# Optimization experiments

Hardware: AMD Instinct MI355X
Metric: run time of the kernel (lower is better)

The kernel has to match this reference:

```python
import jax, jax.numpy as jnp
import numpy as np

BITS = 4
N_PACK = 8  # 32-bit container / 4-bit values
GROUP_SIZE = 128
MASK = (1 << BITS) - 1  # 0xF


def setup_inputs() -> dict:
    key = jax.random.key(0)
    k1, k2, k3, k4, k5 = jax.random.split(key, 5)
    in_f, out_f = 4096, 4096
    tokens = 8192
    n_groups = in_f // GROUP_SIZE
    x = jax.random.normal(k1, (tokens, in_f), dtype=jnp.float32)
    qweight = jax.random.randint(k2, (in_f // N_PACK, out_f), 0, 2147483647, dtype=jnp.int32)
    qzeros = jax.random.randint(k3, (n_groups, out_f // N_PACK), 0, 2147483647, dtype=jnp.int32)
    scales = jax.random.uniform(k4, (n_groups, out_f), dtype=jnp.float32) * 0.01 + 1e-3
    bias = jax.random.normal(k5, (out_f,), dtype=jnp.float32)
    return {"x": x, "qweight": qweight, "qzeros": qzeros, "scales": scales, "bias": bias}


def _unpack_rows(q):
    # q: [in/8, out] int32 -> [in, out] nibbles (unpack along dim 0)
    shifts = (jnp.arange(N_PACK, dtype=jnp.int32) * BITS)  # [8]
    w = (q[:, None, :] >> shifts[None, :, None]) & MASK    # [in/8, 8, out]
    return w.reshape(-1, q.shape[1])                       # [in, out]


def _unpack_cols(q):
    # q: [G, out/8] int32 -> [G, out] nibbles (unpack along dim 1)
    shifts = (jnp.arange(N_PACK, dtype=jnp.int32) * BITS)
    z = (q[:, :, None] >> shifts[None, None, :]) & MASK    # [G, out/8, 8]
    return z.reshape(q.shape[0], -1)                       # [G, out]


def reference(x, qweight, qzeros, scales, bias):
    in_f = qweight.shape[0] * N_PACK
    int_w = _unpack_rows(qweight)                 # [in, out] uint nibbles
    zp = _unpack_cols(qzeros) + 1                 # optimum format: zp was stored as zp-1
    g = jnp.arange(in_f) // GROUP_SIZE            # group index per input channel
    # dequantize: W[i, j] = (int_w[i,j] - zp[g(i), j]) * scales[g(i), j]
    W = (int_w.astype(jnp.float32) - zp[g].astype(jnp.float32)) * scales[g]
    return x @ W + bias
```

## Files before the change

kernel.cpp:

```cpp
#include <hip/hip_runtime.h>
#include <hip/hip_bf16.h>
#include <stdint.h>

typedef __bf16 bf8 __attribute__((ext_vector_type(8)));
typedef float  f4  __attribute__((ext_vector_type(4)));

__device__ __forceinline__ unsigned f2bf(float f) {
  union { float f; unsigned u; } v; v.f = f;
  return (v.u + 0x7FFFu + ((v.u >> 16) & 1u)) >> 16;
}

__device__ __forceinline__ void gload_lds16(const void* g, void* l) {
  __builtin_amdgcn_global_load_lds(
      (const __attribute__((address_space(1))) void*)(uintptr_t)g,
      (__attribute__((address_space(3))) void*)(uint32_t)(uintptr_t)l,
      16, 0, 0);
}

__global__ void cvt_x(const float4* __restrict__ x, uint4* __restrict__ xb, int n16) {
  int i = blockIdx.x * blockDim.x + threadIdx.x;
  if (i >= n16) return;
  float4 f0 = x[2 * i], f1 = x[2 * i + 1];
  uint4 w;
  w.x = f2bf(f0.x) | (f2bf(f0.y) << 16);
  w.y = f2bf(f0.z) | (f2bf(f0.w) << 16);
  w.z = f2bf(f1.x) | (f2bf(f1.y) << 16);
  w.w = f2bf(f1.z) | (f2bf(f1.w) << 16);
  xb[i] = w;
}

__global__ void dq_w(const int* __restrict__ qw, const int* __restrict__ qz,
                     const float* __restrict__ sc, unsigned short* __restrict__ wt,
                     int N, int K, int group_size) {
  int id = blockIdx.x * blockDim.x + threadIdx.x;
  int n  = id % N;
  int kb = id / N;
  if (kb >= K / 64) return;
  int g = (kb * 64) / group_size;
  unsigned zq = ((unsigned)qz[g * (N >> 3) + (n >> 3)] >> (4 * (n & 7))) & 0xFu;
  float zs = (float)(int)(zq + 1u);
  float s  = sc[(size_t)g * N + n];
  #pragma unroll
  for (int r = 0; r < 8; ++r) {
    unsigned q = (unsigned)qw[(size_t)(kb * 8 + r) * N + n];
    uint4 w;
    #pragma unroll
    for (int h = 0; h < 4; ++h) {
      float v0 = (float)(int)((q >> (8 * h))     & 0xFu) - zs;
      float v1 = (float)(int)((q >> (8 * h + 4)) & 0xFu) - zs;
      ((unsigned*)&w)[h] = f2bf(v0 * s) | (f2bf(v1 * s) << 16);
    }
    *(uint4*)(wt + (size_t)n * K + kb * 64 + r * 8) = w;
  }
}

#define BM 256
#define BN 256
#define BK 64

__launch_bounds__(512, 2)
__global__ void gemm_8ph(const unsigned short* __restrict__ A,
                         const unsigned short* __restrict__ B,
                         const float* __restrict__ bias,
                         float* __restrict__ out,
                         int M, int N, int K) {
  __shared__ __align__(16) char smem[131072];

  const int nbx = N / BN;
  const int nwg = (M / BM) * nbx;
  const int id  = blockIdx.y * gridDim.x + blockIdx.x;
  const int cpx = nwg >> 3;
  const int swzid = (id & 7) * cpx + (id >> 3);
  const int m0 = (swzid / nbx) * BM;
  const int n0 = (swzid % nbx) * BN;

  const int t    = threadIdx.x;
  const int wid  = t >> 6, lane = t & 63;
  const int wr   = wid >> 2, wc = wid & 3;
  const int lr   = lane & 15, lk = lane >> 4;
  const unsigned loff = (unsigned)(lr * 64 + (((lk + (lr >> 1)) & 3) << 4));

  const int srow = lane >> 2;
  const int scol = (((lane & 3) - (lane >> 3)) & 3) * 8;

  f4 acc[8][4] = {};

  const int nK = K / BK;

#define STAGE_A(tile, h)                                                          \
  {                                                                               \
    const int _tt = (tile);                                                       \
    _Pragma("unroll")                                                             \
    for (int cg = 0; cg < 2; ++cg) {                                              \
      const unsigned short* _src = A + (size_t)(m0 + (h) * 128 + wid * 16 + srow) * K \
                                     + _tt * BK + cg * 32 + scol;                 \
      char* _dst = smem + (_tt & 1) * 65536 + ((((h) * 8 + wid) * 2 + cg) << 10); \
      gload_lds16(_src, _dst);                                                    \
    }                                                                             \
  }
#define STAGE_B(tile, h)                                                          \
  {                                                                               \
    const int _tt = (tile);                                                       \
    _Pragma("unroll")                                                             \
    for (int cg = 0; cg < 2; ++cg) {                                              \
      const unsigned short* _src = B + (size_t)(n0 + (h) * 128 + wid * 16 + srow) * K \
                                     + _tt * BK + cg * 32 + scol;                 \
      char* _dst = smem + (_tt & 1) * 65536 + 32768 +                             \
                   ((((h) * 8 + wid) * 2 + cg) << 10);                            \
      gload_lds16(_src, _dst);                                                    \
    }                                                                             \
  }

  STAGE_B(0, 0); STAGE_B(0, 1);
  STAGE_A(0, 0); STAGE_A(0, 1);
  if (nK > 1) {
    STAGE_B(1, 0); STAGE_B(1, 1);
    asm volatile("s_waitcnt vmcnt(4)" ::: "memory");
  } else {
    asm volatile("s_waitcnt vmcnt(0)" ::: "memory");
  }
  __builtin_amdgcn_s_barrier();
  __builtin_amdgcn_sched_barrier(0);

  bf8 a[4][2], b[4][2];

  for (int kt = 0; kt < nK; ++kt) {
    const char* pA = smem + (kt & 1) * 65536;
    const char* pB = pA + 32768;
    const int ra = wr * 8;
    const int rb = wc * 4;

    if (kt + 1 < nK) STAGE_A(kt + 1, 0);
    #pragma unroll
    for (int mf = 0; mf < 4; ++mf)
      #pragma unroll
      for (int ks = 0; ks < 2; ++ks)
        a[mf][ks] = *(const bf8*)(pA + (unsigned)((((ra + mf) * 2 + ks) << 10)) + loff);
    #pragma unroll
    for (int nf = 0; nf < 2; ++nf)
      #pragma unroll
      for (int ks = 0; ks < 2; ++ks)
        b[nf][ks] = *(const bf8*)(pB + (unsigned)((((rb + nf) * 2 + ks) << 10)) + loff);
    __builtin_amdgcn_s_barrier();
    __builtin_amdgcn_s_setprio(1);
    #pragma unroll
    for (int mf = 0; mf < 4; ++mf)
      #pragma unroll
      for (int nf = 0; nf < 2; ++nf)
        #pragma unroll
        for (int ks = 0; ks < 2; ++ks)
          acc[mf][nf] = __builtin_amdgcn_mfma_f32_16x16x32_bf16(a[mf][ks], b[nf][ks], acc[mf][nf], 0, 0, 0);
    __builtin_amdgcn_s_setprio(0);
    __builtin_amdgcn_s_barrier();

    if (kt + 1 < nK) STAGE_A(kt + 1, 1);
    #pragma unroll
    for (int nf = 2; nf < 4; ++nf)
      #pragma unroll
      for (int ks = 0; ks < 2; ++ks)
        b[nf][ks] = *(const bf8*)(pB + (unsigned)((((rb + nf) * 2 + ks) << 10)) + loff);
    __builtin_amdgcn_s_barrier();
    __builtin_amdgcn_s_setprio(1);
    #pragma unroll
    for (int mf = 0; mf < 4; ++mf)
      #pragma unroll
      for (int nf = 2; nf < 4; ++nf)
        #pragma unroll
        for (int ks = 0; ks < 2; ++ks)
          acc[mf][nf] = __builtin_amdgcn_mfma_f32_16x16x32_bf16(a[mf][ks], b[nf][ks], acc[mf][nf], 0, 0, 0);
    __builtin_amdgcn_s_setprio(0);
    __builtin_amdgcn_s_barrier();

    if (kt + 2 < nK) STAGE_B(kt + 2, 0);
    #pragma unroll
    for (int mf = 0; mf < 4; ++mf)
      #pragma unroll
      for (int ks = 0; ks < 2; ++ks)
        a[mf][ks] = *(const bf8*)(pA + (unsigned)((((ra + 4 + mf) * 2 + ks) << 10)) + loff);
    __builtin_amdgcn_s_barrier();
    __builtin_amdgcn_s_setprio(1);
    #pragma unroll
    for (int mf = 0; mf < 4; ++mf)
      #pragma unroll
      for (int nf = 2; nf < 4; ++nf)
        #pragma unroll
        for (int ks = 0; ks < 2; ++ks)
          acc[4 + mf][nf] = __builtin_amdgcn_mfma_f32_16x16x32_bf16(a[mf][ks], b[nf][ks], acc[4 + mf][nf], 0, 0, 0);
    __builtin_amdgcn_s_setprio(0);
    __builtin_amdgcn_s_barrier();

    if (kt + 2 < nK) {
      STAGE_B(kt + 2, 1);
      asm volatile("s_waitcnt vmcnt(4)" ::: "memory");
    } else {
      asm volatile("s_waitcnt vmcnt(0)" ::: "memory");
    }
    __builtin_amdgcn_s_barrier();
    __builtin_amdgcn_sched_barrier(0);
    __builtin_amdgcn_s_setprio(1);
    #pragma unroll
    for (int mf = 0; mf < 4; ++mf)
      #pragma unroll
      for (int nf = 0; nf < 2; ++nf)
        #pragma unroll
        for (int ks = 0; ks < 2; ++ks)
          acc[4 + mf][nf] = __builtin_amdgcn_mfma_f32_16x16x32_bf16(a[mf][ks], b[nf][ks], acc[4 + mf][nf], 0, 0, 0);
    __builtin_amdgcn_s_setprio(0);
    __builtin_amdgcn_s_barrier();
  }

  #pragma unroll
  for (int ni = 0; ni < 4; ++ni) {
    int col = n0 + wc * 64 + ni * 16 + lr;
    float bv = bias[col];
    #pragma unroll
    for (int mi = 0; mi < 8; ++mi) {
      int row = m0 + wr * 128 + mi * 16 + lk * 4;
      #pragma unroll
      for (int r = 0; r < 4; ++r)
        out[(size_t)(row + r) * N + col] = acc[mi][ni][r] + bv;
    }
  }
#undef STAGE_A
#undef STAGE_B
}

#define FBM 128
#define FBN 128
#define FBK 64
__launch_bounds__(256, 2)
__global__ void woq_gemm(const float* __restrict__ x,
                         const int*   __restrict__ qweight,
                         const int*   __restrict__ qzeros,
                         const float* __restrict__ scales,
                         const float* __restrict__ bias,
                         float*       __restrict__ out,
                         int M, int N, int K) {
  __shared__ unsigned short sA[FBM * FBK];
  __shared__ unsigned short sB[FBN * FBK];
  const int t = threadIdx.x;
  const int n0 = blockIdx.x * FBN, m0 = blockIdx.y * FBM;
  const int wid = t >> 6, lane = t & 63;
  const int wr = wid >> 1, wc = wid & 1;
  const int lr = lane & 15, lk = lane >> 4;
  f4 acc[4][4] = {};
  const int c = t & 127, rbase = t >> 7;
  const int segA = t & 7, rowbA = t >> 3;
  const int nK = K / FBK;
  for (int kt = 0; kt < nK; ++kt) {
    const int k0 = kt * FBK;
    __syncthreads();
    #pragma unroll
    for (int p = 0; p < 4; ++p) {
      int row = rowbA + p * 32;
      const float4* src = (const float4*)(x + (size_t)(m0 + row) * K + k0 + segA * 8);
      float4 f0 = src[0], f1 = src[1];
      uint4 w;
      w.x = f2bf(f0.x) | (f2bf(f0.y) << 16);
      w.y = f2bf(f0.z) | (f2bf(f0.w) << 16);
      w.z = f2bf(f1.x) | (f2bf(f1.y) << 16);
      w.w = f2bf(f1.z) | (f2bf(f1.w) << 16);
      unsigned off = (unsigned)(row * (FBK * 2) + segA * 16) ^ ((row & 7) << 4);
      *(uint4*)((char*)sA + off) = w;
    }
    {
      const int g = k0 >> 7;
      const unsigned zq = (unsigned)qzeros[g * (N >> 3) + ((n0 + c) >> 3)];
      const int   zp = (int)((zq >> (4 * ((n0 + c) & 7))) & 0xFu) + 1;
      const float sc = scales[(size_t)g * N + n0 + c];
      #pragma unroll
      for (int p = 0; p < 4; ++p) {
        int r = rbase + p * 2;
        unsigned uq = (unsigned)qweight[(size_t)(kt * 8 + r) * N + n0 + c];
        uint4 w;
        #pragma unroll
        for (int h = 0; h < 4; ++h) {
          int v0 = (int)((uq >> (8 * h))     & 0xFu) - zp;
          int v1 = (int)((uq >> (8 * h + 4)) & 0xFu) - zp;
          ((unsigned*)&w)[h] = f2bf((float)v0 * sc) | (f2bf((float)v1 * sc) << 16);
        }
        unsigned off = (unsigned)(c * (FBK * 2) + r * 16) ^ ((c & 7) << 4);
        *(uint4*)((char*)sB + off) = w;
      }
    }
    __syncthreads();
    #pragma unroll
    for (int ks = 0; ks < 2; ++ks) {
      bf8 a[4], b[4];
      #pragma unroll
      for (int mi = 0; mi < 4; ++mi) {
        int row = wr * 64 + mi * 16 + lr;
        unsigned off = (unsigned)(row * (FBK * 2) + ks * 64 + lk * 16) ^ ((row & 7) << 4);
        a[mi] = *(const bf8*)((const char*)sA + off);
      }
      #pragma unroll
      for (int ni = 0; ni < 4; ++ni) {
        int rowN = wc * 64 + ni * 16 + lr;
        unsigned off = (unsigned)(rowN * (FBK * 2) + ks * 64 + lk * 16) ^ ((rowN & 7) << 4);
        b[ni] = *(const bf8*)((const char*)sB + off);
      }
      #pragma unroll
      for (int mi = 0; mi < 4; ++mi)
        #pragma unroll
        for (int ni = 0; ni < 4; ++ni)
          acc[mi][ni] = __builtin_amdgcn_mfma_f32_16x16x32_bf16(a[mi], b[ni], acc[mi][ni], 0, 0, 0);
    }
  }
  #pragma unroll
  for (int ni = 0; ni < 4; ++ni) {
    int col = n0 + wc * 64 + ni * 16 + lr;
    float bv = bias[col];
    #pragma unroll
    for (int mi = 0; mi < 4; ++mi) {
      int row = m0 + wr * 64 + mi * 16 + lk * 4;
      #pragma unroll
      for (int r = 0; r < 4; ++r)
        out[(size_t)(row + r) * N + col] = acc[mi][ni][r] + bv;
    }
  }
}

extern "C" void kernel_launch(void* const* d_in, const int* in_sizes, int n_in,
                              void* d_out, int out_size, void* d_ws, size_t ws_size,
                              hipStream_t stream) {
  const float* x  = (const float*)d_in[0];
  const int*   qw = (const int*)d_in[1];
  const int*   qz = (const int*)d_in[2];
  const float* sc = (const float*)d_in[3];
  const float* bs = (const float*)d_in[4];
  float* out = (float*)d_out;

  const int N = in_sizes[4];
  const int K = (int)(((long long)in_sizes[1] * 8) / N);
  const int M = (int)((long long)in_sizes[0] / K);
  const int n_groups   = (int)((long long)in_sizes[3] / N);
  const int group_size = K / n_groups;

  const size_t need = ((size_t)M * K + (size_t)N * K) * 2;
  if (ws_size >= need && (M % BM) == 0 && (N % BN) == 0 && (K % BK) == 0 &&
      ((M / BM) * (N / BN)) % 8 == 0) {
    unsigned short* xb = (unsigned short*)d_ws;
    unsigned short* wt = xb + (size_t)M * K;

    int n16 = M * K / 8;
    cvt_x<<<(n16 + 255) / 256, 256, 0, stream>>>((const float4*)x, (uint4*)xb, n16);

    int ndq = N * (K / 64);
    dq_w<<<(ndq + 255) / 256, 256, 0, stream>>>(qw, qz, sc, wt, N, K, group_size);

    dim3 grid(N / BN, M / BM);
    gemm_8ph<<<grid, 512, 0, stream>>>(xb, wt, bs, out, M, N, K);
  } else {
    dim3 grid(N / FBN, M / FBM);
    woq_gemm<<<grid, 256, 0, stream>>>(x, qw, qz, sc, bs, out, M, N, K);
  }
}
```

Baseline: 301.6 us.

## Overlap LDS fragment reads with MFMA by prefetching next-phase operands

```diff
diff --git a/kernel.cpp b/kernel.cpp
--- a/kernel.cpp
+++ b/kernel.cpp
@@ -59,11 +59,11 @@
 #define BK 64
 
 __launch_bounds__(512, 2)
-__global__ void gemm_8ph(const unsigned short* __restrict__ A,
-                         const unsigned short* __restrict__ B,
-                         const float* __restrict__ bias,
-                         float* __restrict__ out,
-                         int M, int N, int K) {
+__global__ void gemm_owin(const unsigned short* __restrict__ A,
+                          const unsigned short* __restrict__ B,
+                          const float* __restrict__ bias,
+                          float* __restrict__ out,
+                          int M, int N, int K) {
   __shared__ __align__(16) char smem[131072];
 
   const int nbx = N / BN;
@@ -84,8 +84,11 @@
   const int scol = (((lane & 3) - (lane >> 3)) & 3) * 8;
 
   f4 acc[8][4] = {};
+  bf8 aL[4][2], aH[4][2], b01[2][2], b23[2][2];
 
   const int nK = K / BK;
+  const int ra = wr * 8;
+  const int rb = wc * 4;
 
 #define STAGE_A(tile, h)                                                          \
   {                                                                               \
@@ -110,6 +113,7 @@
       gload_lds16(_src, _dst);                                                    \
     }                                                                             \
   }
+#define RD(p, slot) (*(const bf8*)((p) + ((unsigned)(slot) << 10) + loff))
 
   STAGE_B(0, 0); STAGE_B(0, 1);
   STAGE_A(0, 0); STAGE_A(0, 1);
@@ -121,90 +125,101 @@
   }
   __builtin_amdgcn_s_barrier();
   __builtin_amdgcn_sched_barrier(0);
-
-  bf8 a[4][2], b[4][2];
+  {
+    const char* pA = smem;
+    const char* pB = smem + 32768;
+    #pragma unroll
+    for (int mf = 0; mf < 4; ++mf)
+      #pragma unroll
+      for (int ks = 0; ks < 2; ++ks)
+        aL[mf][ks] = RD(pA, (ra + mf) * 2 + ks);
+    #pragma unroll
+    for (int nf = 0; nf < 2; ++nf)
+      #pragma unroll
+      for (int ks = 0; ks < 2; ++ks)
+        b01[nf][ks] = RD(pB, (rb + nf) * 2 + ks);
+  }
 
   for (int kt = 0; kt < nK; ++kt) {
     const char* pA = smem + (kt & 1) * 65536;
     const char* pB = pA + 32768;
-    const int ra = wr * 8;
-    const int rb = wc * 4;
 
     if (kt + 1 < nK) STAGE_A(kt + 1, 0);
-    #pragma unroll
-    for (int mf = 0; mf < 4; ++mf)
+    __builtin_amdgcn_s_setprio(1);
+    #pragma unroll
+    for (int j = 0; j < 2; ++j)
       #pragma unroll
       for (int ks = 0; ks < 2; ++ks)
-        a[mf][ks] = *(const bf8*)(pA + (unsigned)((((ra + mf) * 2 + ks) << 10)) + loff);
-    #pragma unroll
-    for (int nf = 0; nf < 2; ++nf)
-      #pragma unroll
-      for (int ks = 0; ks < 2; ++ks)
-        b[nf][ks] = *(const bf8*)(pB + (unsigned)((((rb + nf) * 2 + ks) << 10)) + loff);
-    __builtin_amdgcn_s_barrier();
-    __builtin_amdgcn_s_setprio(1);
+        b23[j][ks] = RD(pB, (rb + 2 + j) * 2 + ks);
     #pragma unroll
     for (int mf = 0; mf < 4; ++mf)
       #pragma unroll
       for (int nf = 0; nf < 2; ++nf)
         #pragma unroll
         for (int ks = 0; ks < 2; ++ks)
-          acc[mf][nf] = __builtin_amdgcn_mfma_f32_16x16x32_bf16(a[mf][ks], b[nf][ks], acc[mf][nf], 0, 0, 0);
+          acc[mf][nf] = __builtin_amdgcn_mfma_f32_16x16x32_bf16(aL[mf][ks], b01[nf][ks], acc[mf][nf], 0, 0, 0);
     __builtin_amdgcn_s_setprio(0);
     __builtin_amdgcn_s_barrier();
 
     if (kt + 1 < nK) STAGE_A(kt + 1, 1);
-    #pragma unroll
-    for (int nf = 2; nf < 4; ++nf)
+    __builtin_amdgcn_s_setprio(1);
+    #pragma unroll
+    for (int mf = 0; mf < 4; ++mf)
       #pragma unroll
       for (int ks = 0; ks < 2; ++ks)
-        b[nf][ks] = *(const bf8*)(pB + (unsigned)((((rb + nf) * 2 + ks) << 10)) + loff);
-    __builtin_amdgcn_s_barrier();
-    __builtin_amdgcn_s_setprio(1);
-    #pragma unroll
-    for (int mf = 0; mf < 4; ++mf)
-      #pragma unroll
-      for (int nf = 2; nf < 4; ++nf)
-        #pragma unroll
-        for (int ks = 0; ks < 2; ++ks)
-          acc[mf][nf] = __builtin_amdgcn_mfma_f32_16x16x32_bf16(a[mf][ks], b[nf][ks], acc[mf][nf], 0, 0, 0);
+        aH[mf][ks] = RD(pA, (ra + 4 + mf) * 2 + ks);
+    #pragma unroll
+    for (int mf = 0; mf < 4; ++mf)
+      #pragma unroll
+      for (int j = 0; j < 2; ++j)
+        #pragma unroll
+        for (int ks = 0; ks < 2; ++ks)
+          acc[mf][2 + j] = __builtin_amdgcn_mfma_f32_16x16x32_bf16(aL[mf][ks], b23[j][ks], acc[mf][2 + j], 0, 0, 0);
     __builtin_amdgcn_s_setprio(0);
     __builtin_amdgcn_s_barrier();
 
     if (kt + 2 < nK) STAGE_B(kt + 2, 0);
-    #pragma unroll
-    for (int mf = 0; mf < 4; ++mf)
-      #pragma unroll
-      for (int ks = 0; ks < 2; ++ks)
-        a[mf][ks] = *(const bf8*)(pA + (unsigned)((((ra + 4 + mf) * 2 + ks) << 10)) + loff);
-    __builtin_amdgcn_s_barrier();
     __builtin_amdgcn_s_setprio(1);
     #pragma unroll
     for (int mf = 0; mf < 4; ++mf)
       #pragma unroll
-      for (int nf = 2; nf < 4; ++nf)
-        #pragma unroll
-        for (int ks = 0; ks < 2; ++ks)
-          acc[4 + mf][nf] = __builtin_amdgcn_mfma_f32_16x16x32_bf16(a[mf][ks], b[nf][ks], acc[4 + mf][nf], 0, 0, 0);
+      for (int nf = 0; nf < 2; ++nf)
+        #pragma unroll
+        for (int ks = 0; ks < 2; ++ks)
+          acc[4 + mf][nf] = __builtin_amdgcn_mfma_f32_16x16x32_bf16(aH[mf][ks], b01[nf][ks], acc[4 + mf][nf], 0, 0, 0);
     __builtin_amdgcn_s_setprio(0);
-    __builtin_amdgcn_s_barrier();
 
     if (kt + 2 < nK) {
       STAGE_B(kt + 2, 1);
       asm volatile("s_waitcnt vmcnt(4)" ::: "memory");
-    } else {
+    } else if (kt + 1 < nK) {
       asm volatile("s_waitcnt vmcnt(0)" ::: "memory");
     }
     __builtin_amdgcn_s_barrier();
     __builtin_amdgcn_sched_barrier(0);
+
     __builtin_amdgcn_s_setprio(1);
-    #pragma unroll
-    for (int mf = 0; mf < 4; ++mf)
+    if (kt + 1 < nK) {
+      const char* qA = smem + ((kt + 1) & 1) * 65536;
+      const char* qB = qA + 32768;
+      #pragma unroll
+      for (int mf = 0; mf < 4; ++mf)
+        #pragma unroll
+        for (int ks = 0; ks < 2; ++ks)
+          aL[mf][ks] = RD(qA, (ra + mf) * 2 + ks);
       #pragma unroll
       for (int nf = 0; nf < 2; ++nf)
         #pragma unroll
         for (int ks = 0; ks < 2; ++ks)
-          acc[4 + mf][nf] = __builtin_amdgcn_mfma_f32_16x16x32_bf16(a[mf][ks], b[nf][ks], acc[4 + mf][nf], 0, 0, 0);
+          b01[nf][ks] = RD(qB, (rb + nf) * 2 + ks);
+    }
+    #pragma unroll
+    for (int mf = 0; mf < 4; ++mf)
+      #pragma unroll
+      for (int j = 0; j < 2; ++j)
+        #pragma unroll
+        for (int ks = 0; ks < 2; ++ks)
+          acc[4 + mf][2 + j] = __builtin_amdgcn_mfma_f32_16x16x32_bf16(aH[mf][ks], b23[j][ks], acc[4 + mf][2 + j], 0, 0, 0);
     __builtin_amdgcn_s_setprio(0);
     __builtin_amdgcn_s_barrier();
   }
@@ -223,6 +238,7 @@
   }
 #undef STAGE_A
 #undef STAGE_B
+#undef RD
 }
 
 #define FBM 128
@@ -349,7 +365,7 @@
     dq_w<<<(ndq + 255) / 256, 256, 0, stream>>>(qw, qz, sc, wt, N, K, group_size);
 
     dim3 grid(N / BN, M / BM);
-    gemm_8ph<<<grid, 512, 0, stream>>>(xb, wt, bs, out, M, N, K);
+    gemm_owin<<<grid, 512, 0, stream>>>(xb, wt, bs, out, M, N, K);
   } else {
     dim3 grid(N / FBN, M / FBM);
     woq_gemm<<<grid, 256, 0, stream>>>(x, qw, qz, sc, bs, out, M, N, K);
```

Measured after the change: 290.5 us. -3.7%, faster.

## Switch main GEMM to 32x32x16 MFMA with new LDS layout and interleaved schedule

Applied to the files above, without the earlier changes.

```diff
diff --git a/kernel.cpp b/kernel.cpp
--- a/kernel.cpp
+++ b/kernel.cpp
@@ -2,8 +2,9 @@
 #include <hip/hip_bf16.h>
 #include <stdint.h>
 
-typedef __bf16 bf8 __attribute__((ext_vector_type(8)));
-typedef float  f4  __attribute__((ext_vector_type(4)));
+typedef __bf16 bf8  __attribute__((ext_vector_type(8)));
+typedef float  f4   __attribute__((ext_vector_type(4)));
+typedef float  f16v __attribute__((ext_vector_type(16)));
 
 __device__ __forceinline__ unsigned f2bf(float f) {
   union { float f; unsigned u; } v; v.f = f;
@@ -58,12 +59,16 @@
 #define BN 256
 #define BK 64
 
+#define SGB(mask, n) __builtin_amdgcn_sched_group_barrier((mask), (n), 0)
+#define M_MFMA 0x8
+#define M_DSRD 0x100
+
 __launch_bounds__(512, 2)
-__global__ void gemm_8ph(const unsigned short* __restrict__ A,
-                         const unsigned short* __restrict__ B,
-                         const float* __restrict__ bias,
-                         float* __restrict__ out,
-                         int M, int N, int K) {
+__global__ void gemm32(const unsigned short* __restrict__ A,
+                       const unsigned short* __restrict__ B,
+                       const float* __restrict__ bias,
+                       float* __restrict__ out,
+                       int M, int N, int K) {
   __shared__ __align__(16) char smem[131072];
 
   const int nbx = N / BN;
@@ -77,152 +82,154 @@
   const int t    = threadIdx.x;
   const int wid  = t >> 6, lane = t & 63;
   const int wr   = wid >> 2, wc = wid & 3;
-  const int lr   = lane & 15, lk = lane >> 4;
-  const unsigned loff = (unsigned)(lr * 64 + (((lk + (lr >> 1)) & 3) << 4));
-
-  const int srow = lane >> 2;
-  const int scol = (((lane & 3) - (lane >> 3)) & 3) * 8;
-
-  f4 acc[8][4] = {};
+  const int rr   = lane & 31, hi = lane >> 5;
+
+  unsigned lof[4];
+  #pragma unroll
+  for (int ks = 0; ks < 4; ++ks)
+    lof[ks] = (unsigned)(rr * 128 + (((ks * 2 + hi + rr) & 7) << 4));
+
+  const int sr = lane >> 3;
+  const int sc = ((lane & 7) - sr) & 7;
+
+  f16v acc[4][2] = {};
+  bf8 aL[2][4], aH[2][4], b0[4], b1[4];
 
   const int nK = K / BK;
 
-#define STAGE_A(tile, h)                                                          \
+#define STAGE_A(tile)                                                             \
   {                                                                               \
     const int _tt = (tile);                                                       \
     _Pragma("unroll")                                                             \
-    for (int cg = 0; cg < 2; ++cg) {                                              \
-      const unsigned short* _src = A + (size_t)(m0 + (h) * 128 + wid * 16 + srow) * K \
-                                     + _tt * BK + cg * 32 + scol;                 \
-      char* _dst = smem + (_tt & 1) * 65536 + ((((h) * 8 + wid) * 2 + cg) << 10); \
+    for (int p = 0; p < 4; ++p) {                                                 \
+      const unsigned short* _src = A + (size_t)(m0 + wid * 32 + p * 8 + sr) * K   \
+                                     + _tt * BK + sc * 8;                         \
+      char* _dst = smem + (_tt & 1) * 65536 + wid * 4096 + p * 1024;              \
       gload_lds16(_src, _dst);                                                    \
     }                                                                             \
   }
-#define STAGE_B(tile, h)                                                          \
+#define STAGE_B(tile)                                                             \
   {                                                                               \
     const int _tt = (tile);                                                       \
     _Pragma("unroll")                                                             \
-    for (int cg = 0; cg < 2; ++cg) {                                              \
-      const unsigned short* _src = B + (size_t)(n0 + (h) * 128 + wid * 16 + srow) * K \
-                                     + _tt * BK + cg * 32 + scol;                 \
-      char* _dst = smem + (_tt & 1) * 65536 + 32768 +                             \
-                   ((((h) * 8 + wid) * 2 + cg) << 10);                            \
+    for (int p = 0; p < 4; ++p) {                                                 \
+      const unsigned short* _src = B + (size_t)(n0 + wid * 32 + p * 8 + sr) * K   \
+                                     + _tt * BK + sc * 8;                         \
+      char* _dst = smem + (_tt & 1) * 65536 + 32768 + wid * 4096 + p * 1024;      \
       gload_lds16(_src, _dst);                                                    \
     }                                                                             \
   }
-
-  STAGE_B(0, 0); STAGE_B(0, 1);
-  STAGE_A(0, 0); STAGE_A(0, 1);
+#define RD_A(buf, m, ks) (*(const bf8*)(smem + (buf) * 65536 + ((wr * 4 + (m)) << 12) + lof[ks]))
+#define RD_B(buf, n, ks) (*(const bf8*)(smem + (buf) * 65536 + 32768 + ((wc * 2 + (n)) << 12) + lof[ks]))
+
+  STAGE_A(0); STAGE_B(0);
   if (nK > 1) {
-    STAGE_B(1, 0); STAGE_B(1, 1);
+    STAGE_B(1);
     asm volatile("s_waitcnt vmcnt(4)" ::: "memory");
   } else {
     asm volatile("s_waitcnt vmcnt(0)" ::: "memory");
   }
   __builtin_amdgcn_s_barrier();
   __builtin_amdgcn_sched_barrier(0);
-
-  bf8 a[4][2], b[4][2];
+  #pragma unroll
+  for (int m = 0; m < 2; ++m)
+    #pragma unroll
+    for (int ks = 0; ks < 4; ++ks)
+      aL[m][ks] = RD_A(0, m, ks);
+  #pragma unroll
+  for (int ks = 0; ks < 4; ++ks)
+    b0[ks] = RD_B(0, 0, ks);
 
   for (int kt = 0; kt < nK; ++kt) {
-    const char* pA = smem + (kt & 1) * 65536;
-    const char* pB = pA + 32768;
-    const int ra = wr * 8;
-    const int rb = wc * 4;
-
-    if (kt + 1 < nK) STAGE_A(kt + 1, 0);
-    #pragma unroll
-    for (int mf = 0; mf < 4; ++mf)
-      #pragma unroll
-      for (int ks = 0; ks < 2; ++ks)
-        a[mf][ks] = *(const bf8*)(pA + (unsigned)((((ra + mf) * 2 + ks) << 10)) + loff);
-    #pragma unroll
-    for (int nf = 0; nf < 2; ++nf)
-      #pragma unroll
-      for (int ks = 0; ks < 2; ++ks)
-        b[nf][ks] = *(const bf8*)(pB + (unsigned)((((rb + nf) * 2 + ks) << 10)) + loff);
-    __builtin_amdgcn_s_barrier();
+    const int buf  = kt & 1;
+    const int nbuf = ((kt + 1 < nK) ? (kt + 1) : kt) & 1;
+
+    if (kt + 1 < nK) STAGE_A(kt + 1);
     __builtin_amdgcn_s_setprio(1);
     #pragma unroll
-    for (int mf = 0; mf < 4; ++mf)
-      #pragma unroll
-      for (int nf = 0; nf < 2; ++nf)
-        #pragma unroll
-        for (int ks = 0; ks < 2; ++ks)
-          acc[mf][nf] = __builtin_amdgcn_mfma_f32_16x16x32_bf16(a[mf][ks], b[nf][ks], acc[mf][nf], 0, 0, 0);
+    for (int ks = 0; ks < 4; ++ks)
+      b1[ks] = RD_B(buf, 1, ks);
+    #pragma unroll
+    for (int ks = 0; ks < 4; ++ks)
+      #pragma unroll
+      for (int m = 0; m < 2; ++m)
+        acc[m][0] = __builtin_amdgcn_mfma_f32_32x32x16_bf16(aL[m][ks], b0[ks], acc[m][0], 0, 0, 0);
+    #pragma unroll
+    for (int r = 0; r < 4; ++r) { SGB(M_DSRD, 1); SGB(M_MFMA, 2); }
     __builtin_amdgcn_s_setprio(0);
     __builtin_amdgcn_s_barrier();
 
-    if (kt + 1 < nK) STAGE_A(kt + 1, 1);
-    #pragma unroll
-    for (int nf = 2; nf < 4; ++nf)
-      #pragma unroll
-      for (int ks = 0; ks < 2; ++ks)
-        b[nf][ks] = *(const bf8*)(pB + (unsigned)((((rb + nf) * 2 + ks) << 10)) + loff);
-    __builtin_amdgcn_s_barrier();
     __builtin_amdgcn_s_setprio(1);
     #pragma unroll
-    for (int mf = 0; mf < 4; ++mf)
-      #pragma unroll
-      for (int nf = 2; nf < 4; ++nf)
-        #pragma unroll
-        for (int ks = 0; ks < 2; ++ks)
-          acc[mf][nf] = __builtin_amdgcn_mfma_f32_16x16x32_bf16(a[mf][ks], b[nf][ks], acc[mf][nf], 0, 0, 0);
+    for (int m = 0; m < 2; ++m)
+      #pragma unroll
+      for (int ks = 0; ks < 4; ++ks)
+        aH[m][ks] = RD_A(buf, 2 + m, ks);
+    #pragma unroll
+    for (int ks = 0; ks < 4; ++ks)
+      #pragma unroll
+      for (int m = 0; m < 2; ++m)
+        acc[m][1] = __builtin_amdgcn_mfma_f32_32x32x16_bf16(aL[m][ks], b1[ks], acc[m][1], 0, 0, 0);
+    #pragma unroll
+    for (int r = 0; r < 4; ++r) { SGB(M_DSRD, 2); SGB(M_MFMA, 2); }
     __builtin_amdgcn_s_setprio(0);
     __builtin_amdgcn_s_barrier();
 
-    if (kt + 2 < nK) STAGE_B(kt + 2, 0);
-    #pragma unroll
-    for (int mf = 0; mf < 4; ++mf)
-      #pragma unroll
-      for (int ks = 0; ks < 2; ++ks)
-        a[mf][ks] = *(const bf8*)(pA + (unsigned)((((ra + 4 + mf) * 2 + ks) << 10)) + loff);
-    __builtin_amdgcn_s_barrier();
+    if (kt + 2 < nK) STAGE_B(kt + 2);
     __builtin_amdgcn_s_setprio(1);
     #pragma unroll
-    for (int mf = 0; mf < 4; ++mf)
-      #pragma unroll
-      for (int nf = 2; nf < 4; ++nf)
-        #pragma unroll
-        for (int ks = 0; ks < 2; ++ks)
-          acc[4 + mf][nf] = __builtin_amdgcn_mfma_f32_16x16x32_bf16(a[mf][ks], b[nf][ks], acc[4 + mf][nf], 0, 0, 0);
+    for (int ks = 0; ks < 4; ++ks)
+      #pragma unroll
+      for (int m = 0; m < 2; ++m)
+        acc[2 + m][0] = __builtin_amdgcn_mfma_f32_32x32x16_bf16(aH[m][ks], b0[ks], acc[2 + m][0], 0, 0, 0);
+    SGB(M_MFMA, 8);
     __builtin_amdgcn_s_setprio(0);
-    __builtin_amdgcn_s_barrier();
-
     if (kt + 2 < nK) {
-      STAGE_B(kt + 2, 1);
       asm volatile("s_waitcnt vmcnt(4)" ::: "memory");
     } else {
       asm volatile("s_waitcnt vmcnt(0)" ::: "memory");
     }
     __builtin_amdgcn_s_barrier();
     __builtin_amdgcn_sched_barrier(0);
+
     __builtin_amdgcn_s_setprio(1);
     #pragma unroll
-    for (int mf = 0; mf < 4; ++mf)
-      #pragma unroll
-      for (int nf = 0; nf < 2; ++nf)
-        #pragma unroll
-        for (int ks = 0; ks < 2; ++ks)
-          acc[4 + mf][nf] = __builtin_amdgcn_mfma_f32_16x16x32_bf16(a[mf][ks], b[nf][ks], acc[4 + mf][nf], 0, 0, 0);
+    for (int m = 0; m < 2; ++m)
+      #pragma unroll
+      for (int ks = 0; ks < 4; ++ks)
+        aL[m][ks] = RD_A(nbuf, m, ks);
+    #pragma unroll
+    for (int ks = 0; ks < 4; ++ks)
+      b0[ks] = RD_B(nbuf, 0, ks);
+    #pragma unroll
+    for (int ks = 0; ks < 4; ++ks)
+      #pragma unroll
+      for (int m = 0; m < 2; ++m)
+        acc[2 + m][1] = __builtin_amdgcn_mfma_f32_32x32x16_bf16(aH[m][ks], b1[ks], acc[2 + m][1], 0, 0, 0);
+    #pragma unroll
+    for (int r = 0; r < 4; ++r) { SGB(M_DSRD, 3); SGB(M_MFMA, 2); }
     __builtin_amdgcn_s_setprio(0);
     __builtin_amdgcn_s_barrier();
   }
 
   #pragma unroll
-  for (int ni = 0; ni < 4; ++ni) {
-    int col = n0 + wc * 64 + ni * 16 + lr;
+  for (int nf = 0; nf < 2; ++nf) {
+    int col = n0 + wc * 64 + nf * 32 + rr;
     float bv = bias[col];
     #pragma unroll
-    for (int mi = 0; mi < 8; ++mi) {
-      int row = m0 + wr * 128 + mi * 16 + lk * 4;
-      #pragma unroll
-      for (int r = 0; r < 4; ++r)
-        out[(size_t)(row + r) * N + col] = acc[mi][ni][r] + bv;
+    for (int mf = 0; mf < 4; ++mf) {
+      int rowb = m0 + wr * 128 + mf * 32 + 4 * hi;
+      #pragma unroll
+      for (int reg = 0; reg < 16; ++reg) {
+        int row = rowb + (reg & 3) + 8 * (reg >> 2);
+        out[(size_t)row * N + col] = acc[mf][nf][reg] + bv;
+      }
     }
   }
 #undef STAGE_A
 #undef STAGE_B
+#undef RD_A
+#undef RD_B
 }
 
 #define FBM 128
@@ -267,7 +274,7 @@
       const int g = k0 >> 7;
       const unsigned zq = (unsigned)qzeros[g * (N >> 3) + ((n0 + c) >> 3)];
       const int   zp = (int)((zq >> (4 * ((n0 + c) & 7))) & 0xFu) + 1;
-      const float sc = scales[(size_t)g * N + n0 + c];
+      const float sc2 = scales[(size_t)g * N + n0 + c];
       #pragma unroll
       for (int p = 0; p < 4; ++p) {
         int r = rbase + p * 2;
@@ -277,7 +284,7 @@
         for (int h = 0; h < 4; ++h) {
           int v0 = (int)((uq >> (8 * h))     & 0xFu) - zp;
           int v1 = (int)((uq >> (8 * h + 4)) & 0xFu) - zp;
-          ((unsigned*)&w)[h] = f2bf((float)v0 * sc) | (f2bf((float)v1 * sc) << 16);
+          ((unsigned*)&w)[h] = f2bf((float)v0 * sc2) | (f2bf((float)v1 * sc2) << 16);
         }
         unsigned off = (unsigned)(c * (FBK * 2) + r * 16) ^ ((c & 7) << 4);
         *(uint4*)((char*)sB + off) = w;
@@ -349,7 +356,7 @@
     dq_w<<<(ndq + 255) / 256, 256, 0, stream>>>(qw, qz, sc, wt, N, K, group_size);
 
     dim3 grid(N / BN, M / BM);
-    gemm_8ph<<<grid, 512, 0, stream>>>(xb, wt, bs, out, M, N, K);
+    gemm32<<<grid, 512, 0, stream>>>(xb, wt, bs, out, M, N, K);
   } else {
     dim3 grid(N / FBN, M / FBM);
     woq_gemm<<<grid, 256, 0, stream>>>(x, qw, qz, sc, bs, out, M, N, K);
```

Measured after the change: 310.3 us. +2.9%, slower.

## Restructure GEMM main loop into four phases with separate A/B fragment registers

Applied to the files above, without the earlier changes.

```diff
diff --git a/kernel.cpp b/kernel.cpp
--- a/kernel.cpp
+++ b/kernel.cpp
@@ -59,11 +59,11 @@
 #define BK 64
 
 __launch_bounds__(512, 2)
-__global__ void gemm_8ph(const unsigned short* __restrict__ A,
-                         const unsigned short* __restrict__ B,
-                         const float* __restrict__ bias,
-                         float* __restrict__ out,
-                         int M, int N, int K) {
+__global__ void gemm_m201(const unsigned short* __restrict__ A,
+                          const unsigned short* __restrict__ B,
+                          const float* __restrict__ bias,
+                          float* __restrict__ out,
+                          int M, int N, int K) {
   __shared__ __align__(16) char smem[131072];
 
   const int nbx = N / BN;
@@ -84,8 +84,11 @@
   const int scol = (((lane & 3) - (lane >> 3)) & 3) * 8;
 
   f4 acc[8][4] = {};
+  bf8 aL[4][2], aH[4][2], b0[2][2], b1[2][2];
 
   const int nK = K / BK;
+  const int ra = wr * 8;
+  const int rb = wc * 4;
 
 #define STAGE_A(tile, h)                                                          \
   {                                                                               \
@@ -110,11 +113,11 @@
       gload_lds16(_src, _dst);                                                    \
     }                                                                             \
   }
-
-  STAGE_B(0, 0); STAGE_B(0, 1);
-  STAGE_A(0, 0); STAGE_A(0, 1);
+#define RD(p, slot) (*(const bf8*)((p) + ((unsigned)(slot) << 10) + loff))
+
+  STAGE_A(0, 0); STAGE_B(0, 0); STAGE_B(0, 1); STAGE_A(0, 1);
   if (nK > 1) {
-    STAGE_B(1, 0); STAGE_B(1, 1);
+    STAGE_A(1, 0); STAGE_B(1, 0);
     asm volatile("s_waitcnt vmcnt(4)" ::: "memory");
   } else {
     asm volatile("s_waitcnt vmcnt(0)" ::: "memory");
@@ -122,80 +125,24 @@
   __builtin_amdgcn_s_barrier();
   __builtin_amdgcn_sched_barrier(0);
 
-  bf8 a[4][2], b[4][2];
-
   for (int kt = 0; kt < nK; ++kt) {
     const char* pA = smem + (kt & 1) * 65536;
     const char* pB = pA + 32768;
-    const int ra = wr * 8;
-    const int rb = wc * 4;
-
-    if (kt + 1 < nK) STAGE_A(kt + 1, 0);
+
     #pragma unroll
     for (int mf = 0; mf < 4; ++mf)
       #pragma unroll
       for (int ks = 0; ks < 2; ++ks)
-        a[mf][ks] = *(const bf8*)(pA + (unsigned)((((ra + mf) * 2 + ks) << 10)) + loff);
+        aL[mf][ks] = RD(pA, (ra + mf) * 2 + ks);
     #pragma unroll
     for (int nf = 0; nf < 2; ++nf)
       #pragma unroll
       for (int ks = 0; ks < 2; ++ks)
-        b[nf][ks] = *(const bf8*)(pB + (unsigned)((((rb + nf) * 2 + ks) << 10)) + loff);
-    __builtin_amdgcn_s_barrier();
-    __builtin_amdgcn_s_setprio(1);
-    #pragma unroll
-    for (int mf = 0; mf < 4; ++mf)
-      #pragma unroll
-      for (int nf = 0; nf < 2; ++nf)
-        #pragma unroll
-        for (int ks = 0; ks < 2; ++ks)
-          acc[mf][nf] = __builtin_amdgcn_mfma_f32_16x16x32_bf16(a[mf][ks], b[nf][ks], acc[mf][nf], 0, 0, 0);
-    __builtin_amdgcn_s_setprio(0);
-    __builtin_amdgcn_s_barrier();
-
-    if (kt + 1 < nK) STAGE_A(kt + 1, 1);
-    #pragma unroll
-    for (int nf = 2; nf < 4; ++nf)
-      #pragma unroll
-      for (int ks = 0; ks < 2; ++ks)
-        b[nf][ks] = *(const bf8*)(pB + (unsigned)((((rb + nf) * 2 + ks) << 10)) + loff);
-    __builtin_amdgcn_s_barrier();
-    __builtin_amdgcn_s_setprio(1);
-    #pragma unroll
-    for (int mf = 0; mf < 4; ++mf)
-      #pragma unroll
-      for (int nf = 2; nf < 4; ++nf)
-        #pragma unroll
-        for (int ks = 0; ks < 2; ++ks)
-          acc[mf][nf] = __builtin_amdgcn_mfma_f32_16x16x32_bf16(a[mf][ks], b[nf][ks], acc[mf][nf], 0, 0, 0);
-    __builtin_amdgcn_s_setprio(0);
-    __builtin_amdgcn_s_barrier();
-
-    if (kt + 2 < nK) STAGE_B(kt + 2, 0);
-    #pragma unroll
-    for (int mf = 0; mf < 4; ++mf)
-      #pragma unroll
-      for (int ks = 0; ks < 2; ++ks)
-        a[mf][ks] = *(const bf8*)(pA + (unsigned)((((ra + 4 + mf) * 2 + ks) << 10)) + loff);
-    __builtin_amdgcn_s_barrier();
-    __builtin_amdgcn_s_setprio(1);
-    #pragma unroll
-    for (int mf = 0; mf < 4; ++mf)
-      #pragma unroll
-      for (int nf = 2; nf < 4; ++nf)
-        #pragma unroll
-        for (int ks = 0; ks < 2; ++ks)
-          acc[4 + mf][nf] = __builtin_amdgcn_mfma_f32_16x16x32_bf16(a[mf][ks], b[nf][ks], acc[4 + mf][nf], 0, 0, 0);
-    __builtin_amdgcn_s_setprio(0);
-    __builtin_amdgcn_s_barrier();
-
-    if (kt + 2 < nK) {
-      STAGE_B(kt + 2, 1);
-      asm volatile("s_waitcnt vmcnt(4)" ::: "memory");
-    } else {
-      asm volatile("s_waitcnt vmcnt(0)" ::: "memory");
-    }
-    __builtin_amdgcn_s_barrier();
+        b0[nf][ks] = RD(pB, (rb + nf) * 2 + ks);
+    if (kt + 1 < nK) STAGE_B(kt + 1, 1);
+    asm volatile("s_waitcnt lgkmcnt(8)" ::: "memory");
+    __builtin_amdgcn_s_barrier();
+    asm volatile("s_waitcnt lgkmcnt(0)" ::: "memory");
     __builtin_amdgcn_sched_barrier(0);
     __builtin_amdgcn_s_setprio(1);
     #pragma unroll
@@ -204,9 +151,70 @@
       for (int nf = 0; nf < 2; ++nf)
         #pragma unroll
         for (int ks = 0; ks < 2; ++ks)
-          acc[4 + mf][nf] = __builtin_amdgcn_mfma_f32_16x16x32_bf16(a[mf][ks], b[nf][ks], acc[4 + mf][nf], 0, 0, 0);
+          acc[mf][nf] = __builtin_amdgcn_mfma_f32_16x16x32_bf16(aL[mf][ks], b0[nf][ks], acc[mf][nf], 0, 0, 0);
     __builtin_amdgcn_s_setprio(0);
     __builtin_amdgcn_s_barrier();
+
+    #pragma unroll
+    for (int nf = 0; nf < 2; ++nf)
+      #pragma unroll
+      for (int ks = 0; ks < 2; ++ks)
+        b1[nf][ks] = RD(pB, (rb + 2 + nf) * 2 + ks);
+    if (kt + 1 < nK) STAGE_A(kt + 1, 1);
+    __builtin_amdgcn_s_barrier();
+    asm volatile("s_waitcnt lgkmcnt(0)" ::: "memory");
+    __builtin_amdgcn_sched_barrier(0);
+    __builtin_amdgcn_s_setprio(1);
+    #pragma unroll
+    for (int mf = 0; mf < 4; ++mf)
+      #pragma unroll
+      for (int nf = 0; nf < 2; ++nf)
+        #pragma unroll
+        for (int ks = 0; ks < 2; ++ks)
+          acc[mf][2 + nf] = __builtin_amdgcn_mfma_f32_16x16x32_bf16(aL[mf][ks], b1[nf][ks], acc[mf][2 + nf], 0, 0, 0);
+    __builtin_amdgcn_s_setprio(0);
+    __builtin_amdgcn_s_barrier();
+
+    #pragma unroll
+    for (int mf = 0; mf < 4; ++mf)
+      #pragma unroll
+      for (int ks = 0; ks < 2; ++ks)
+        aH[mf][ks] = RD(pA, (ra + 4 + mf) * 2 + ks);
+    if (kt + 2 < nK) STAGE_A(kt + 2, 0);
+    __builtin_amdgcn_s_barrier();
+    asm volatile("s_waitcnt lgkmcnt(0)" ::: "memory");
+    __builtin_amdgcn_sched_barrier(0);
+    __builtin_amdgcn_s_setprio(1);
+    #pragma unroll
+    for (int mf = 0; mf < 4; ++mf)
+      #pragma unroll
+      for (int nf = 0; nf < 2; ++nf)
+        #pragma unroll
+        for (int ks = 0; ks < 2; ++ks)
+          acc[4 + mf][nf] = __builtin_amdgcn_mfma_f32_16x16x32_bf16(aH[mf][ks], b0[nf][ks], acc[4 + mf][nf], 0, 0, 0);
+    __builtin_amdgcn_s_setprio(0);
+    __builtin_amdgcn_s_barrier();
+
+    if (kt + 2 < nK) STAGE_B(kt + 2, 0);
+    __builtin_amdgcn_s_barrier();
+    __builtin_amdgcn_s_setprio(1);
+    #pragma unroll
+    for (int mf = 0; mf < 4; ++mf)
+      #pragma unroll
+      for (int nf = 0; nf < 2; ++nf)
+        #pragma unroll
+        for (int ks = 0; ks < 2; ++ks)
+          acc[4 + mf][2 + nf] = __builtin_amdgcn_mfma_f32_16x16x32_bf16(aH[mf][ks], b1[nf][ks], acc[4 + mf][2 + nf], 0, 0, 0);
+    __builtin_amdgcn_s_setprio(0);
+    if (kt + 1 < nK) {
+      if (kt + 2 < nK) {
+        asm volatile("s_waitcnt vmcnt(4)" ::: "memory");
+      } else {
+        asm volatile("s_waitcnt vmcnt(0)" ::: "memory");
+      }
+    }
+    __builtin_amdgcn_s_barrier();
+    __builtin_amdgcn_sched_barrier(0);
   }
 
   #pragma unroll
@@ -223,6 +231,7 @@
   }
 #undef STAGE_A
 #undef STAGE_B
+#undef RD
 }
 
 #define FBM 128
@@ -267,7 +276,7 @@
       const int g = k0 >> 7;
       const unsigned zq = (unsigned)qzeros[g * (N >> 3) + ((n0 + c) >> 3)];
       const int   zp = (int)((zq >> (4 * ((n0 + c) & 7))) & 0xFu) + 1;
-      const float sc = scales[(size_t)g * N + n0 + c];
+      const float sc2 = scales[(size_t)g * N + n0 + c];
       #pragma unroll
       for (int p = 0; p < 4; ++p) {
         int r = rbase + p * 2;
@@ -277,7 +286,7 @@
         for (int h = 0; h < 4; ++h) {
           int v0 = (int)((uq >> (8 * h))     & 0xFu) - zp;
           int v1 = (int)((uq >> (8 * h + 4)) & 0xFu) - zp;
-          ((unsigned*)&w)[h] = f2bf((float)v0 * sc) | (f2bf((float)v1 * sc) << 16);
+          ((unsigned*)&w)[h] = f2bf((float)v0 * sc2) | (f2bf((float)v1 * sc2) << 16);
         }
         unsigned off = (unsigned)(c * (FBK * 2) + r * 16) ^ ((c & 7) << 4);
         *(uint4*)((char*)sB + off) = w;
@@ -349,7 +358,7 @@
     dq_w<<<(ndq + 255) / 256, 256, 0, stream>>>(qw, qz, sc, wt, N, K, group_size);
 
     dim3 grid(N / BN, M / BM);
-    gemm_8ph<<<grid, 512, 0, stream>>>(xb, wt, bs, out, M, N, K);
+    gemm_m201<<<grid, 512, 0, stream>>>(xb, wt, bs, out, M, N, K);
   } else {
     dim3 grid(N / FBN, M / FBM);
     woq_gemm<<<grid, 256, 0, stream>>>(x, qw, qz, sc, bs, out, M, N, K);
```

After: 301.2 us. Within noise of the previous version (-0.2%).
